# Kernel optimization log

Measured on AMD Instinct MI355X. Metric: run time of the kernel, lower is better.

The kernel has to match this reference:

```python
import jax, jax.numpy as jnp
import numpy as np

NUM_EXPERTS = 8
TOP_K = 2
HIDDEN = 1024
INTER = 3584
TOKENS = 16384


def setup_inputs() -> dict:
    key = jax.random.key(0)
    k0, k1, k2, k3, k4 = jax.random.split(key, 5)
    s = 0.02
    return {
        "hidden_states": jax.random.normal(k0, (TOKENS, HIDDEN), dtype=jnp.float32),
        "gate_w": jax.random.normal(k1, (NUM_EXPERTS, HIDDEN), dtype=jnp.float32) * s,
        "w1": jax.random.normal(k2, (NUM_EXPERTS, INTER, HIDDEN), dtype=jnp.float32) * s,
        "w3": jax.random.normal(k3, (NUM_EXPERTS, INTER, HIDDEN), dtype=jnp.float32) * s,
        "w2": jax.random.normal(k4, (NUM_EXPERTS, HIDDEN, INTER), dtype=jnp.float32) * s,
    }


def reference(hidden_states, gate_w, w1, w3, w2):
    # Router: logits -> softmax -> top-k -> renormalize (Mixtral gating)
    router_logits = jnp.einsum("th,eh->te", hidden_states, gate_w)  # [T, E]
    probs = jax.nn.softmax(router_logits, axis=-1)
    topk_w, topk_idx = jax.lax.top_k(probs, TOP_K)                  # [T, K]
    topk_w = topk_w / jnp.sum(topk_w, axis=-1, keepdims=True)
    # Dense combine weights: [T, E], zero for unselected experts
    combine = jnp.sum(
        jax.nn.one_hot(topk_idx, NUM_EXPERTS, dtype=hidden_states.dtype)
        * topk_w[..., None],
        axis=1,
    )
    out = jnp.zeros_like(hidden_states)
    for e in range(NUM_EXPERTS):  # small fixed expert loop
        h = jnp.einsum("th,ih->ti", hidden_states, w1[e])   # gate proj
        u = jnp.einsum("th,ih->ti", hidden_states, w3[e])   # up proj
        act = jax.nn.silu(h) * u                             # SwiGLU
        y = jnp.einsum("ti,hi->th", act, w2[e])              # down proj
        out = out + combine[:, e:e + 1] * y
    return out
```

## Files before the change

### kernel.cpp

```cpp
#include <hip/hip_runtime.h>
#include <hip/hip_bf16.h>

#define T_TOKENS 16384
#define HID 1024
#define NEXP 8
#define INTER 3584
#define PAIRS (2*T_TOKENS)
#define PAD_MAX (PAIRS + NEXP*256)

using f32x4    = __attribute__((ext_vector_type(4))) float;
using bfrag    = __attribute__((ext_vector_type(8))) short;
using float4_t = __attribute__((ext_vector_type(4))) float;
using ushort8_t = __attribute__((ext_vector_type(8))) unsigned short;

__device__ inline unsigned short f2bf(float f){
    unsigned u = __float_as_uint(f);
    u += 0x7FFFu + ((u >> 16) & 1u);
    return (unsigned short)(u >> 16);
}

__device__ inline void gload16(const unsigned short* g, unsigned short* l){
    __builtin_amdgcn_global_load_lds(
        (const __attribute__((address_space(1))) void*)g,
        (__attribute__((address_space(3))) void*)l, 16, 0, 0);
}

#define BAR_VM8() asm volatile("s_waitcnt vmcnt(8)\n\ts_barrier" ::: "memory")
#define BAR_VM4() asm volatile("s_waitcnt vmcnt(4)\n\ts_barrier" ::: "memory")
#define BAR_VM0() asm volatile("s_waitcnt vmcnt(0)\n\ts_barrier" ::: "memory")
#define BAR_PLAIN() asm volatile("s_barrier" ::: "memory")

__device__ inline int xcd_swz(int flat, int nwg){
    int q = nwg >> 3, r = nwg & 7;
    int xcd = flat & 7, idx = flat >> 3;
    return (xcd < r ? xcd*(q+1) : r*(q+1) + (xcd - r)*q) + idx;
}

__device__ inline void st_decode(int sw, int nM, int nP, int STM,
                                 int& mt, int& p){
    int stSize = STM * nP;
    int st = sw / stSize;
    int rem = sw - st * stSize;
    int base = st * STM;
    int stM = (base + STM <= nM) ? STM : (nM - base);
    p  = rem / stM;
    mt = base + (rem - p * stM);
}

__global__ __launch_bounds__(256) void conv3_kernel(
    const float* __restrict__ w1, const float* __restrict__ w3,
    const float* __restrict__ w2,
    unsigned short* __restrict__ w1b, unsigned short* __restrict__ w3b,
    unsigned short* __restrict__ w2b)
{
    const int n = NEXP * INTER * HID;
    const float* in = (blockIdx.y == 0) ? w1 : (blockIdx.y == 1) ? w3 : w2;
    unsigned short* out = (blockIdx.y == 0) ? w1b : (blockIdx.y == 1) ? w3b : w2b;
    int i0 = (blockIdx.x * 256 + threadIdx.x) * 8;
    int stride = gridDim.x * 256 * 8;
    for (int i = i0; i < n; i += stride){
        float4_t a = *reinterpret_cast<const float4_t*>(in + i);
        float4_t b = *reinterpret_cast<const float4_t*>(in + i + 4);
        ushort8_t o;
        o[0]=f2bf(a.x); o[1]=f2bf(a.y); o[2]=f2bf(a.z); o[3]=f2bf(a.w);
        o[4]=f2bf(b.x); o[5]=f2bf(b.y); o[6]=f2bf(b.z); o[7]=f2bf(b.w);
        *reinterpret_cast<ushort8_t*>(out + i) = o;
    }
}

__global__ __launch_bounds__(256) void router_kernel(
    const float* __restrict__ x, const float* __restrict__ gw,
    int* __restrict__ topk_idx, float* __restrict__ topk_w,
    unsigned short* __restrict__ xb)
{
    int wave = threadIdx.x >> 6;
    int lane = threadIdx.x & 63;
    int t = blockIdx.x * 4 + wave;

    float acc[NEXP];
#pragma unroll
    for (int e = 0; e < NEXP; ++e) acc[e] = 0.f;

    const float* xr = x + (size_t)t * HID;
    for (int hb = 0; hb < HID; hb += 64){
        float xv = xr[hb + lane];
#pragma unroll
        for (int e = 0; e < NEXP; ++e)
            acc[e] += xv * gw[e * HID + hb + lane];
    }

    unsigned short* xbr = xb + (size_t)t * HID;
#pragma unroll
    for (int r = 0; r < 2; ++r){
        int c = (lane + r*64) * 8;
        float4_t va = *reinterpret_cast<const float4_t*>(xr + c);
        float4_t vb = *reinterpret_cast<const float4_t*>(xr + c + 4);
        ushort8_t o;
        o[0]=f2bf(va.x); o[1]=f2bf(va.y); o[2]=f2bf(va.z); o[3]=f2bf(va.w);
        o[4]=f2bf(vb.x); o[5]=f2bf(vb.y); o[6]=f2bf(vb.z); o[7]=f2bf(vb.w);
        *reinterpret_cast<ushort8_t*>(xbr + c) = o;
    }

#pragma unroll
    for (int e = 0; e < NEXP; ++e){
#pragma unroll
        for (int s = 32; s > 0; s >>= 1)
            acc[e] += __shfl_xor(acc[e], s, 64);
    }
    if (lane == 0){
        int e0 = 0; float m0 = acc[0];
#pragma unroll
        for (int e = 1; e < NEXP; ++e) if (acc[e] > m0){ m0 = acc[e]; e0 = e; }
        int e1 = -1; float m1 = -1e30f;
#pragma unroll
        for (int e = 0; e < NEXP; ++e) if (e != e0 && acc[e] > m1){ m1 = acc[e]; e1 = e; }
        float p1 = __expf(m1 - m0);
        float inv = 1.f / (1.f + p1);
        topk_idx[2*t]   = e0;
        topk_idx[2*t+1] = e1;
        topk_w[2*t]   = inv;
        topk_w[2*t+1] = p1 * inv;
    }
}

__global__ __launch_bounds__(256) void hist_kernel(
    const int* __restrict__ topk_idx, int* __restrict__ counts)
{
    __shared__ int h[NEXP];
    if (threadIdx.x < NEXP) h[threadIdx.x] = 0;
    __syncthreads();
    int i0 = blockIdx.x * 256 + threadIdx.x;
    for (int i = i0; i < PAIRS; i += gridDim.x * 256)
        atomicAdd(&h[topk_idx[i]], 1);
    __syncthreads();
    if (threadIdx.x < NEXP) atomicAdd(&counts[threadIdx.x], h[threadIdx.x]);
}

__global__ void scan_kernel(const int* __restrict__ counts, int* __restrict__ offp)
{
    if (threadIdx.x == 0 && blockIdx.x == 0){
        int s = 0;
        for (int e = 0; e < NEXP; ++e){
            offp[e] = s;
            s += (counts[e] + 255) & ~255;
        }
        offp[NEXP] = s;
    }
}

__global__ __launch_bounds__(128) void padfill_kernel(
    const int* __restrict__ counts, const int* __restrict__ offp,
    int* __restrict__ pair_token, float* __restrict__ pair_w)
{
    int e = blockIdx.x;
    int base = offp[e];
    int aligned = offp[e+1] - base;
    for (int s = counts[e] + threadIdx.x; s < aligned; s += 128){
        pair_token[base + s] = (base + s) & (T_TOKENS - 1);
        pair_w[base + s] = 0.f;
    }
}

__global__ __launch_bounds__(256) void scatter_kernel(
    const int* __restrict__ topk_idx, const float* __restrict__ topk_w,
    const int* __restrict__ offp, int* __restrict__ cursors,
    int* __restrict__ pair_token, float* __restrict__ pair_w)
{
    __shared__ int hist[NEXP], base[NEXP], lcur[NEXP];
    int tid = threadIdx.x;
    if (tid < NEXP){ hist[tid] = 0; lcur[tid] = 0; }
    __syncthreads();

    int t = blockIdx.x * 256 + tid;
    int e0 = topk_idx[2*t], e1 = topk_idx[2*t + 1];
    atomicAdd(&hist[e0], 1);
    atomicAdd(&hist[e1], 1);
    __syncthreads();

    if (tid < NEXP) base[tid] = atomicAdd(&cursors[tid], hist[tid]);
    __syncthreads();

    int r0 = atomicAdd(&lcur[e0], 1);
    int r1 = atomicAdd(&lcur[e1], 1);
    int p0 = offp[e0] + base[e0] + r0;
    int p1 = offp[e1] + base[e1] + r1;
    pair_token[p0] = t;  pair_w[p0] = topk_w[2*t];
    pair_token[p1] = t;  pair_w[p1] = topk_w[2*t + 1];
}

__global__ __launch_bounds__(512) void gemm_act_kernel(
    const unsigned short* __restrict__ xb,
    const unsigned short* __restrict__ w1b,
    const unsigned short* __restrict__ w3b,
    const int* __restrict__ offp,
    const int* __restrict__ pair_token, const float* __restrict__ pair_w,
    unsigned short* __restrict__ act, int r0)
{
    int nP = gridDim.x, nM = gridDim.y;
    int sw = xcd_swz(blockIdx.y * nP + blockIdx.x, nP * nM);
    int mt, p;
    st_decode(sw, nM, nP, 4, mt, p);
    int by = mt, bx = p;

    int R = r0 + by * 256;
    if (R >= offp[NEXP]) return;
    int e = 0;
    while (offp[e+1] <= R) ++e;
    int icol0 = bx * 128;

    __shared__ alignas(16) unsigned short As0s[256*64], B1s0[128*64], B3s0[128*64];
    __shared__ alignas(16) unsigned short As1s[256*64], B1s1[128*64], B3s1[128*64];
    __shared__ int   toks[256];
    __shared__ float pws[256];

    int tid = threadIdx.x;
    if (tid < 256){
        toks[tid] = pair_token[R + tid];
        pws[tid]  = pair_w[R + tid];
    }
    __syncthreads();

    int w = tid >> 6, lane = tid & 63;
    int wm = w >> 2, wn = w & 3;
    int l15 = lane & 15;
    int sr = tid >> 3;
    int swzc8 = ((tid & 7) ^ (sr & 7)) * 8;

    const unsigned short* w1e = w1b + (size_t)e * INTER * HID;
    const unsigned short* w3e = w3b + (size_t)e * INTER * HID;

    size_t asrc[2][2];
#pragma unroll
    for (int h = 0; h < 2; ++h)
#pragma unroll
        for (int g = 0; g < 2; ++g)
            asrc[h][g] = (size_t)toks[h*128 + g*64 + sr] * HID + swzc8;
    size_t boff[2];
#pragma unroll
    for (int g = 0; g < 2; ++g)
        boff[g] = (size_t)(icol0 + g*64 + sr) * HID + swzc8;

    int ccol[2];
#pragma unroll
    for (int kk = 0; kk < 2; ++kk)
        ccol[kk] = (((kk*4 + (lane >> 4)) ^ (lane & 7)) * 8);

    f32x4 acc[8][4];
#pragma unroll
    for (int m = 0; m < 8; ++m)
#pragma unroll
        for (int n = 0; n < 4; ++n)
            acc[m][n] = (f32x4){0.f,0.f,0.f,0.f};

    bfrag asub[4][2];
    bfrag bsub[2][2];

    auto stA = [&](unsigned short* As, int h, int t){
        int kc = t * 64;
        gload16(xb + asrc[h][0] + kc, As + h*8192 + tid*8);
        gload16(xb + asrc[h][1] + kc, As + h*8192 + 4096 + tid*8);
    };
    auto stBh = [&](unsigned short* B1s, int t){
        int kc = t * 64;
        gload16(w1e + boff[0] + kc, B1s + tid*8);
        gload16(w1e + boff[1] + kc, B1s + 4096 + tid*8);
    };
    auto stBu = [&](unsigned short* B3s, int t){
        int kc = t * 64;
        gload16(w3e + boff[0] + kc, B3s + tid*8);
        gload16(w3e + boff[1] + kc, B3s + 4096 + tid*8);
    };

    auto dsA = [&](const unsigned short* As, int Mh){
#pragma unroll
        for (int mfl = 0; mfl < 4; ++mfl)
#pragma unroll
            for (int kk = 0; kk < 2; ++kk)
                asub[mfl][kk] = *reinterpret_cast<const bfrag*>(
                    &As[(Mh*128 + wm*64 + mfl*16 + l15)*64 + ccol[kk]]);
    };
    auto dsB = [&](const unsigned short* Bs){
#pragma unroll
        for (int nf = 0; nf < 2; ++nf)
#pragma unroll
            for (int kk = 0; kk < 2; ++kk)
                bsub[nf][kk] = *reinterpret_cast<const bfrag*>(
                    &Bs[(wn*32 + nf*16 + l15)*64 + ccol[kk]]);
    };
    auto mma = [&](int Mh, int S){
        __builtin_amdgcn_s_setprio(1);
#pragma unroll
        for (int kk = 0; kk < 2; ++kk)
#pragma unroll
            for (int nf = 0; nf < 2; ++nf)
#pragma unroll
                for (int mfl = 0; mfl < 4; ++mfl)
                    acc[Mh*4+mfl][S*2+nf] = __builtin_amdgcn_mfma_f32_16x16x32_bf16(
                        asub[mfl][kk], bsub[nf][kk], acc[Mh*4+mfl][S*2+nf], 0, 0, 0);
        __builtin_amdgcn_s_setprio(0);
    };

    const int NT = HID / 64;

    stBh(B1s0, 0);
    stA(As0s, 1, 0);
    stA(As0s, 0, 0);
    stBu(B3s0, 0);
    stBh(B1s1, 1);
    stA(As1s, 1, 1);
    BAR_VM4();

#pragma unroll 1
    for (int i = 0; i < NT/2 - 1; ++i){
        int t1 = 2*i + 1, t2 = 2*i + 2, t3 = 2*i + 3;
        dsA(As0s, 0); dsB(B1s0);
        stA(As1s, 0, t1);
        BAR_PLAIN(); mma(0, 0); BAR_PLAIN();
        dsA(As0s, 1);
        stBu(B3s1, t1);
        BAR_PLAIN(); mma(1, 0); BAR_PLAIN();
        dsB(B3s0);
        stBh(B1s0, t2);
        BAR_PLAIN(); mma(1, 1); BAR_PLAIN();
        dsA(As0s, 0);
        stA(As0s, 1, t2);
        BAR_VM4(); mma(0, 1); BAR_PLAIN();
        dsA(As1s, 0); dsB(B1s1);
        stA(As0s, 0, t2);
        BAR_PLAIN(); mma(0, 0); BAR_PLAIN();
        dsA(As1s, 1);
        stBu(B3s0, t2);
        BAR_PLAIN(); mma(1, 0); BAR_PLAIN();
        dsB(B3s1);
        stBh(B1s1, t3);
        BAR_PLAIN(); mma(1, 1); BAR_PLAIN();
        dsA(As1s, 0);
        stA(As1s, 1, t3);
        BAR_VM4(); mma(0, 1); BAR_PLAIN();
    }

    dsA(As0s, 0); dsB(B1s0);
    stA(As1s, 0, NT-1);
    BAR_PLAIN(); mma(0, 0); BAR_PLAIN();
    dsA(As0s, 1);
    stBu(B3s1, NT-1);
    BAR_PLAIN(); mma(1, 0); BAR_PLAIN();
    dsB(B3s0);
    BAR_PLAIN(); mma(1, 1); BAR_PLAIN();
    dsA(As0s, 0);
    BAR_VM0(); mma(0, 1); BAR_PLAIN();
    dsA(As1s, 0); dsB(B1s1);
    BAR_PLAIN(); mma(0, 0); BAR_PLAIN();
    dsA(As1s, 1);
    BAR_PLAIN(); mma(1, 0); BAR_PLAIN();
    dsB(B3s1);
    BAR_PLAIN(); mma(1, 1); BAR_PLAIN();
    dsA(As1s, 0);
    BAR_PLAIN(); mma(0, 1); BAR_PLAIN();

    size_t arow0 = (size_t)(by * 256) * INTER;
#pragma unroll
    for (int m = 0; m < 8; ++m){
#pragma unroll
        for (int nf = 0; nf < 2; ++nf){
#pragma unroll
            for (int j = 0; j < 4; ++j){
                int rl = (m >> 2)*128 + wm*64 + (m & 3)*16 + (lane >> 4)*4 + j;
                float h = acc[m][nf][j];
                float u = acc[m][2 + nf][j];
                float v = pws[rl] * h * u / (1.f + __expf(-h));
                int ic = icol0 + wn*32 + nf*16 + l15;
                act[arow0 + (size_t)rl * INTER + ic] = f2bf(v);
            }
        }
    }
}

__global__ __launch_bounds__(256) void gemm2_kernel(
    const unsigned short* __restrict__ act,
    const unsigned short* __restrict__ w2b,
    const int* __restrict__ offp,
    const int* __restrict__ pair_token,
    float* __restrict__ out, int r0)
{
    int nP = gridDim.x, nM = gridDim.y;
    int sw = xcd_swz(blockIdx.y * nP + blockIdx.x, nP * nM);
    int mt, p;
    st_decode(sw, nM, nP, 4, mt, p);
    int by = mt, bx = p;

    int R = r0 + by * 128;
    if (R >= offp[NEXP]) return;
    int e = 0;
    while (offp[e+1] <= R) ++e;
    int h0 = bx * 128;

    __shared__ alignas(16) unsigned short As0[128*64], As1[128*64];
    __shared__ alignas(16) unsigned short Bs0[128*64], Bs1[128*64];
    __shared__ int toks[128];

    int tid = threadIdx.x;
    if (tid < 128) toks[tid] = pair_token[R + tid];
    __syncthreads();

    int w = tid >> 6, lane = tid & 63;
    int wm = w >> 1, wn = w & 1;
    int lr = lane >> 3;
    int l15 = lane & 15;
    int swz8 = ((lane & 7) ^ lr) * 8;

    const unsigned short* w2e = w2b + (size_t)e * HID * INTER;
    size_t arow0 = (size_t)(by * 128) * INTER;

    size_t asrc[4], bsrc[4];
#pragma unroll
    for (int i = 0; i < 4; ++i){
        asrc[i] = arow0 + (size_t)(w*32 + i*8 + lr) * INTER + swz8;
        bsrc[i] = (size_t)(h0 + w*32 + i*8 + lr) * INTER + swz8;
    }

    int ccol[2];
#pragma unroll
    for (int kk = 0; kk < 2; ++kk)
        ccol[kk] = (((kk*4 + (lane >> 4)) ^ (lane & 7)) * 8);

    f32x4 acc[4][4];
#pragma unroll
    for (int m = 0; m < 4; ++m)
#pragma unroll
        for (int n = 0; n < 4; ++n)
            acc[m][n] = (f32x4){0.f,0.f,0.f,0.f};

    auto stageT = [&](unsigned short* As, unsigned short* Bs, int t){
        int kc = t * 64;
#pragma unroll
        for (int i = 0; i < 4; ++i) gload16(act + asrc[i] + kc, As + (w*32 + i*8)*64);
#pragma unroll
        for (int i = 0; i < 4; ++i) gload16(w2e + bsrc[i] + kc, Bs + (w*32 + i*8)*64);
    };

    auto computeT = [&](const unsigned short* As, const unsigned short* Bs){
        __builtin_amdgcn_s_setprio(1);
#pragma unroll
        for (int kk = 0; kk < 2; ++kk){
            int cc = ccol[kk];
            bfrag a[4];
#pragma unroll
            for (int m = 0; m < 4; ++m)
                a[m] = *reinterpret_cast<const bfrag*>(&As[(wm*64 + m*16 + l15)*64 + cc]);
#pragma unroll
            for (int n = 0; n < 4; ++n){
                bfrag b = *reinterpret_cast<const bfrag*>(&Bs[(wn*64 + n*16 + l15)*64 + cc]);
#pragma unroll
                for (int m = 0; m < 4; ++m)
                    acc[m][n] = __builtin_amdgcn_mfma_f32_16x16x32_bf16(a[m], b, acc[m][n], 0, 0, 0);
            }
        }
        __builtin_amdgcn_s_setprio(0);
    };

    const int NT = INTER / 64;
    stageT(As0, Bs0, 0);
    stageT(As1, Bs1, 1);
#pragma unroll 1
    for (int t = 0; t < NT - 2; t += 2){
        BAR_VM8();
        computeT(As0, Bs0);
        BAR_PLAIN();
        stageT(As0, Bs0, t + 2);
        BAR_VM8();
        computeT(As1, Bs1);
        BAR_PLAIN();
        stageT(As1, Bs1, t + 3);
    }
    BAR_VM8();
    computeT(As0, Bs0);
    BAR_VM0();
    computeT(As1, Bs1);

#pragma unroll
    for (int m = 0; m < 4; ++m){
#pragma unroll
        for (int n = 0; n < 4; ++n){
#pragma unroll
            for (int j = 0; j < 4; ++j){
                int rl = wm*64 + m*16 + (lane >> 4)*4 + j;
                int hc = h0 + wn*64 + n*16 + l15;
                atomicAdd(&out[(size_t)toks[rl] * HID + hc], acc[m][n][j]);
            }
        }
    }
}

extern "C" void kernel_launch(void* const* d_in, const int* in_sizes, int n_in,
                              void* d_out, int out_size, void* d_ws, size_t ws_size,
                              hipStream_t stream)
{
    const float* x  = (const float*)d_in[0];
    const float* gw = (const float*)d_in[1];
    const float* w1 = (const float*)d_in[2];
    const float* w3 = (const float*)d_in[3];
    const float* w2 = (const float*)d_in[4];
    float* out = (float*)d_out;

    char* ws = (char*)d_ws;
    size_t off = 0;
    auto bump = [&](size_t bytes) -> void* {
        void* p = ws + off;
        off = (off + bytes + 255) & ~(size_t)255;
        return p;
    };
    int*   counts     = (int*)bump(32);
    int*   cursors    = (int*)bump(32);
    int*   offp       = (int*)bump(64);
    int*   topk_idx   = (int*)bump((size_t)PAIRS * 4);
    float* topk_w     = (float*)bump((size_t)PAIRS * 4);
    int*   pair_token = (int*)bump((size_t)PAD_MAX * 4);
    float* pair_w     = (float*)bump((size_t)PAD_MAX * 4);
    unsigned short* xb  = (unsigned short*)bump((size_t)T_TOKENS * HID * 2);
    unsigned short* w1b = (unsigned short*)bump((size_t)NEXP * INTER * HID * 2);
    unsigned short* w3b = (unsigned short*)bump((size_t)NEXP * INTER * HID * 2);
    unsigned short* w2b = (unsigned short*)bump((size_t)NEXP * HID * INTER * 2);
    unsigned short* act = (unsigned short*)(ws + off);

    size_t rem = (ws_size > off) ? (ws_size - off) : 0;
    int RC = (int)(rem / ((size_t)INTER * 2));
    RC &= ~255;
    if (RC > PAD_MAX) RC = PAD_MAX;
    if (RC < 256) RC = 256;
    int nchunks = (PAD_MAX + RC - 1) / RC;

    hipMemsetAsync(d_out, 0, (size_t)T_TOKENS * HID * 4, stream);
    hipMemsetAsync(ws, 0, 1024, stream);

    conv3_kernel<<<dim3(768, 3), 256, 0, stream>>>(w1, w3, w2, w1b, w3b, w2b);

    router_kernel<<<T_TOKENS/4, 256, 0, stream>>>(x, gw, topk_idx, topk_w, xb);
    hist_kernel<<<64, 256, 0, stream>>>(topk_idx, counts);
    scan_kernel<<<1, 64, 0, stream>>>(counts, offp);
    padfill_kernel<<<NEXP, 128, 0, stream>>>(counts, offp, pair_token, pair_w);
    scatter_kernel<<<T_TOKENS/256, 256, 0, stream>>>(topk_idx, topk_w, offp, cursors,
                                                     pair_token, pair_w);

    for (int c = 0; c < nchunks; ++c){
        int r0 = c * RC;
        gemm_act_kernel<<<dim3(INTER/128, RC/256), 512, 0, stream>>>(
            xb, w1b, w3b, offp, pair_token, pair_w, act, r0);
        gemm2_kernel<<<dim3(HID/128, RC/128), 256, 0, stream>>>(
            act, w2b, offp, pair_token, out, r0);
    }
}
```

Before: 1.089 ms.

## Triple-buffer both MoE GEMMs and retile gemm2 to 256-row 512-thread blocks

The gate/up GEMM now uses 256x64 output tiles, with the h and u accumulators kept separate. Its K-loop runs a three-stage LDS ring with a uniform per-tile schedule instead of the hand-interleaved double-buffer sequence. The down-projection GEMM moves from 128x128 tiles with 256 threads to 256x128 tiles with 512 threads and the same three-stage ring, which halves the number of row blocks reloading W2. Deeper prefetch is meant to hide global-load latency better, at the cost of more LDS per block (lower occupancy) and, for the first GEMM, twice as many column blocks re-reading the gathered activations.

```diff
diff --git a/kernel.cpp b/kernel.cpp
--- a/kernel.cpp
+++ b/kernel.cpp
@@ -25,8 +25,7 @@
         (__attribute__((address_space(3))) void*)l, 16, 0, 0);
 }
 
-#define BAR_VM8() asm volatile("s_waitcnt vmcnt(8)\n\ts_barrier" ::: "memory")
-#define BAR_VM4() asm volatile("s_waitcnt vmcnt(4)\n\ts_barrier" ::: "memory")
+#define BAR_VM6() asm volatile("s_waitcnt vmcnt(6)\n\ts_barrier" ::: "memory")
 #define BAR_VM0() asm volatile("s_waitcnt vmcnt(0)\n\ts_barrier" ::: "memory")
 #define BAR_PLAIN() asm volatile("s_barrier" ::: "memory")
 
@@ -206,10 +205,11 @@
     if (R >= offp[NEXP]) return;
     int e = 0;
     while (offp[e+1] <= R) ++e;
-    int icol0 = bx * 128;
-
-    __shared__ alignas(16) unsigned short As0s[256*64], B1s0[128*64], B3s0[128*64];
-    __shared__ alignas(16) unsigned short As1s[256*64], B1s1[128*64], B3s1[128*64];
+    int icol0 = bx * 64;
+
+    __shared__ alignas(16) unsigned short A0[256*64], A1[256*64], A2[256*64];
+    __shared__ alignas(16) unsigned short B10[64*64], B11[64*64], B12[64*64];
+    __shared__ alignas(16) unsigned short B30[64*64], B31[64*64], B32[64*64];
     __shared__ int   toks[256];
     __shared__ float pws[256];
 
@@ -235,148 +235,105 @@
 #pragma unroll
         for (int g = 0; g < 2; ++g)
             asrc[h][g] = (size_t)toks[h*128 + g*64 + sr] * HID + swzc8;
-    size_t boff[2];
-#pragma unroll
-    for (int g = 0; g < 2; ++g)
-        boff[g] = (size_t)(icol0 + g*64 + sr) * HID + swzc8;
+    size_t bsrc = (size_t)(icol0 + sr) * HID + swzc8;
 
     int ccol[2];
 #pragma unroll
     for (int kk = 0; kk < 2; ++kk)
         ccol[kk] = (((kk*4 + (lane >> 4)) ^ (lane & 7)) * 8);
 
-    f32x4 acc[8][4];
-#pragma unroll
-    for (int m = 0; m < 8; ++m)
-#pragma unroll
-        for (int n = 0; n < 4; ++n)
-            acc[m][n] = (f32x4){0.f,0.f,0.f,0.f};
+    f32x4 acc_h[8], acc_u[8];
+#pragma unroll
+    for (int m = 0; m < 8; ++m){
+        acc_h[m] = (f32x4){0.f,0.f,0.f,0.f};
+        acc_u[m] = (f32x4){0.f,0.f,0.f,0.f};
+    }
 
     bfrag asub[4][2];
-    bfrag bsub[2][2];
-
-    auto stA = [&](unsigned short* As, int h, int t){
-        int kc = t * 64;
-        gload16(xb + asrc[h][0] + kc, As + h*8192 + tid*8);
-        gload16(xb + asrc[h][1] + kc, As + h*8192 + 4096 + tid*8);
-    };
-    auto stBh = [&](unsigned short* B1s, int t){
-        int kc = t * 64;
-        gload16(w1e + boff[0] + kc, B1s + tid*8);
-        gload16(w1e + boff[1] + kc, B1s + 4096 + tid*8);
-    };
-    auto stBu = [&](unsigned short* B3s, int t){
-        int kc = t * 64;
-        gload16(w3e + boff[0] + kc, B3s + tid*8);
-        gload16(w3e + boff[1] + kc, B3s + 4096 + tid*8);
-    };
-
-    auto dsA = [&](const unsigned short* As, int Mh){
-#pragma unroll
-        for (int mfl = 0; mfl < 4; ++mfl)
+    bfrag bh[2], bu[2];
+
+    auto stA = [&](unsigned short* A, int h, int t){
+        int k0 = t * 64;
+        gload16(xb + asrc[h][0] + k0, A + h*8192 + tid*8);
+        gload16(xb + asrc[h][1] + k0, A + h*8192 + 4096 + tid*8);
+    };
+    auto stB = [&](unsigned short* B1, unsigned short* B3, int t){
+        int k0 = t * 64;
+        gload16(w1e + bsrc + k0, B1 + tid*8);
+        gload16(w3e + bsrc + k0, B3 + tid*8);
+    };
+
+    auto dsA = [&](const unsigned short* A, int q){
+#pragma unroll
+        for (int i = 0; i < 4; ++i)
 #pragma unroll
             for (int kk = 0; kk < 2; ++kk)
-                asub[mfl][kk] = *reinterpret_cast<const bfrag*>(
-                    &As[(Mh*128 + wm*64 + mfl*16 + l15)*64 + ccol[kk]]);
-    };
-    auto dsB = [&](const unsigned short* Bs){
-#pragma unroll
-        for (int nf = 0; nf < 2; ++nf)
-#pragma unroll
-            for (int kk = 0; kk < 2; ++kk)
-                bsub[nf][kk] = *reinterpret_cast<const bfrag*>(
-                    &Bs[(wn*32 + nf*16 + l15)*64 + ccol[kk]]);
-    };
-    auto mma = [&](int Mh, int S){
+                asub[i][kk] = *reinterpret_cast<const bfrag*>(
+                    &A[(wm*128 + q*64 + i*16 + l15)*64 + ccol[kk]]);
+    };
+    auto dsB = [&](const unsigned short* B1, const unsigned short* B3){
+#pragma unroll
+        for (int kk = 0; kk < 2; ++kk){
+            bh[kk] = *reinterpret_cast<const bfrag*>(&B1[(wn*16 + l15)*64 + ccol[kk]]);
+            bu[kk] = *reinterpret_cast<const bfrag*>(&B3[(wn*16 + l15)*64 + ccol[kk]]);
+        }
+    };
+    auto mma = [&](int q){
         __builtin_amdgcn_s_setprio(1);
 #pragma unroll
         for (int kk = 0; kk < 2; ++kk)
 #pragma unroll
-            for (int nf = 0; nf < 2; ++nf)
-#pragma unroll
-                for (int mfl = 0; mfl < 4; ++mfl)
-                    acc[Mh*4+mfl][S*2+nf] = __builtin_amdgcn_mfma_f32_16x16x32_bf16(
-                        asub[mfl][kk], bsub[nf][kk], acc[Mh*4+mfl][S*2+nf], 0, 0, 0);
+            for (int i = 0; i < 4; ++i){
+                acc_h[q*4+i] = __builtin_amdgcn_mfma_f32_16x16x32_bf16(asub[i][kk], bh[kk], acc_h[q*4+i], 0, 0, 0);
+                acc_u[q*4+i] = __builtin_amdgcn_mfma_f32_16x16x32_bf16(asub[i][kk], bu[kk], acc_u[q*4+i], 0, 0, 0);
+            }
         __builtin_amdgcn_s_setprio(0);
     };
 
-    const int NT = HID / 64;
-
-    stBh(B1s0, 0);
-    stA(As0s, 1, 0);
-    stA(As0s, 0, 0);
-    stBu(B3s0, 0);
-    stBh(B1s1, 1);
-    stA(As1s, 1, 1);
-    BAR_VM4();
+    auto TILE = [&](const unsigned short* Xa, const unsigned short* Xb1, const unsigned short* Xb3,
+                    unsigned short* Ya, unsigned short* Yb1, unsigned short* Yb3,
+                    int tn, int mode){
+        dsA(Xa, 0); dsB(Xb1, Xb3);
+        if (mode == 0){ stA(Ya, 0, tn); stA(Ya, 1, tn); }
+        BAR_PLAIN(); mma(0); BAR_PLAIN();
+        dsA(Xa, 1);
+        if (mode == 0) stB(Yb1, Yb3, tn);
+        if (mode == 0) BAR_VM6();
+        else if (mode == 1) BAR_VM0();
+        else BAR_PLAIN();
+        mma(1); BAR_PLAIN();
+    };
+
+    stA(A0, 0, 0); stA(A0, 1, 0); stB(B10, B30, 0);
+    stA(A1, 0, 1); stA(A1, 1, 1); stB(B11, B31, 1);
+    BAR_VM6();
 
 #pragma unroll 1
-    for (int i = 0; i < NT/2 - 1; ++i){
-        int t1 = 2*i + 1, t2 = 2*i + 2, t3 = 2*i + 3;
-        dsA(As0s, 0); dsB(B1s0);
-        stA(As1s, 0, t1);
-        BAR_PLAIN(); mma(0, 0); BAR_PLAIN();
-        dsA(As0s, 1);
-        stBu(B3s1, t1);
-        BAR_PLAIN(); mma(1, 0); BAR_PLAIN();
-        dsB(B3s0);
-        stBh(B1s0, t2);
-        BAR_PLAIN(); mma(1, 1); BAR_PLAIN();
-        dsA(As0s, 0);
-        stA(As0s, 1, t2);
-        BAR_VM4(); mma(0, 1); BAR_PLAIN();
-        dsA(As1s, 0); dsB(B1s1);
-        stA(As0s, 0, t2);
-        BAR_PLAIN(); mma(0, 0); BAR_PLAIN();
-        dsA(As1s, 1);
-        stBu(B3s0, t2);
-        BAR_PLAIN(); mma(1, 0); BAR_PLAIN();
-        dsB(B3s1);
-        stBh(B1s1, t3);
-        BAR_PLAIN(); mma(1, 1); BAR_PLAIN();
-        dsA(As1s, 0);
-        stA(As1s, 1, t3);
-        BAR_VM4(); mma(0, 1); BAR_PLAIN();
-    }
-
-    dsA(As0s, 0); dsB(B1s0);
-    stA(As1s, 0, NT-1);
-    BAR_PLAIN(); mma(0, 0); BAR_PLAIN();
-    dsA(As0s, 1);
-    stBu(B3s1, NT-1);
-    BAR_PLAIN(); mma(1, 0); BAR_PLAIN();
-    dsB(B3s0);
-    BAR_PLAIN(); mma(1, 1); BAR_PLAIN();
-    dsA(As0s, 0);
-    BAR_VM0(); mma(0, 1); BAR_PLAIN();
-    dsA(As1s, 0); dsB(B1s1);
-    BAR_PLAIN(); mma(0, 0); BAR_PLAIN();
-    dsA(As1s, 1);
-    BAR_PLAIN(); mma(1, 0); BAR_PLAIN();
-    dsB(B3s1);
-    BAR_PLAIN(); mma(1, 1); BAR_PLAIN();
-    dsA(As1s, 0);
-    BAR_PLAIN(); mma(0, 1); BAR_PLAIN();
+    for (int g = 0; g < 4; ++g){
+        TILE(A0, B10, B30, A2, B12, B32, 3*g + 2, 0);
+        TILE(A1, B11, B31, A0, B10, B30, 3*g + 3, 0);
+        TILE(A2, B12, B32, A1, B11, B31, 3*g + 4, 0);
+    }
+    TILE(A0, B10, B30, A2, B12, B32, 14, 0);
+    TILE(A1, B11, B31, A0, B10, B30, 15, 0);
+    TILE(A2, B12, B32, A0, B10, B30, 0, 1);
+    TILE(A0, B10, B30, A0, B10, B30, 0, 2);
 
     size_t arow0 = (size_t)(by * 256) * INTER;
 #pragma unroll
     for (int m = 0; m < 8; ++m){
 #pragma unroll
-        for (int nf = 0; nf < 2; ++nf){
-#pragma unroll
-            for (int j = 0; j < 4; ++j){
-                int rl = (m >> 2)*128 + wm*64 + (m & 3)*16 + (lane >> 4)*4 + j;
-                float h = acc[m][nf][j];
-                float u = acc[m][2 + nf][j];
-                float v = pws[rl] * h * u / (1.f + __expf(-h));
-                int ic = icol0 + wn*32 + nf*16 + l15;
-                act[arow0 + (size_t)rl * INTER + ic] = f2bf(v);
-            }
+        for (int j = 0; j < 4; ++j){
+            int rl = wm*128 + m*16 + (lane >> 4)*4 + j;
+            float h = acc_h[m][j];
+            float u = acc_u[m][j];
+            float v = pws[rl] * h * u / (1.f + __expf(-h));
+            act[arow0 + (size_t)rl * INTER + icol0 + wn*16 + l15] = f2bf(v);
         }
     }
 }
 
-__global__ __launch_bounds__(256) void gemm2_kernel(
+__global__ __launch_bounds__(512) void gemm2_kernel(
     const unsigned short* __restrict__ act,
     const unsigned short* __restrict__ w2b,
     const int* __restrict__ offp,
@@ -386,107 +343,133 @@
     int nP = gridDim.x, nM = gridDim.y;
     int sw = xcd_swz(blockIdx.y * nP + blockIdx.x, nP * nM);
     int mt, p;
-    st_decode(sw, nM, nP, 4, mt, p);
+    st_decode(sw, nM, nP, 2, mt, p);
     int by = mt, bx = p;
 
-    int R = r0 + by * 128;
+    int R = r0 + by * 256;
     if (R >= offp[NEXP]) return;
     int e = 0;
     while (offp[e+1] <= R) ++e;
     int h0 = bx * 128;
 
-    __shared__ alignas(16) unsigned short As0[128*64], As1[128*64];
-    __shared__ alignas(16) unsigned short Bs0[128*64], Bs1[128*64];
-    __shared__ int toks[128];
+    __shared__ alignas(16) unsigned short A0[256*64], A1[256*64], A2[256*64];
+    __shared__ alignas(16) unsigned short B0[128*64], B1[128*64], B2[128*64];
+    __shared__ int toks[256];
 
     int tid = threadIdx.x;
-    if (tid < 128) toks[tid] = pair_token[R + tid];
+    if (tid < 256) toks[tid] = pair_token[R + tid];
     __syncthreads();
 
     int w = tid >> 6, lane = tid & 63;
-    int wm = w >> 1, wn = w & 1;
-    int lr = lane >> 3;
+    int wm = w >> 2, wn = w & 3;
     int l15 = lane & 15;
-    int swz8 = ((lane & 7) ^ lr) * 8;
+    int sr = tid >> 3;
+    int swzc8 = ((tid & 7) ^ (sr & 7)) * 8;
 
     const unsigned short* w2e = w2b + (size_t)e * HID * INTER;
-    size_t arow0 = (size_t)(by * 128) * INTER;
-
-    size_t asrc[4], bsrc[4];
-#pragma unroll
-    for (int i = 0; i < 4; ++i){
-        asrc[i] = arow0 + (size_t)(w*32 + i*8 + lr) * INTER + swz8;
-        bsrc[i] = (size_t)(h0 + w*32 + i*8 + lr) * INTER + swz8;
-    }
+    size_t arow0 = (size_t)(by * 256) * INTER;
+
+    size_t asrc[2][2];
+#pragma unroll
+    for (int h = 0; h < 2; ++h)
+#pragma unroll
+        for (int g = 0; g < 2; ++g)
+            asrc[h][g] = arow0 + (size_t)(h*128 + g*64 + sr) * INTER + swzc8;
+    size_t bsrc[2];
+#pragma unroll
+    for (int g = 0; g < 2; ++g)
+        bsrc[g] = (size_t)(h0 + g*64 + sr) * INTER + swzc8;
 
     int ccol[2];
 #pragma unroll
     for (int kk = 0; kk < 2; ++kk)
         ccol[kk] = (((kk*4 + (lane >> 4)) ^ (lane & 7)) * 8);
 
-    f32x4 acc[4][4];
-#pragma unroll
-    for (int m = 0; m < 4; ++m)
-#pragma unroll
-        for (int n = 0; n < 4; ++n)
+    f32x4 acc[8][2];
+#pragma unroll
+    for (int m = 0; m < 8; ++m)
+#pragma unroll
+        for (int n = 0; n < 2; ++n)
             acc[m][n] = (f32x4){0.f,0.f,0.f,0.f};
 
-    auto stageT = [&](unsigned short* As, unsigned short* Bs, int t){
+    bfrag asub[4][2];
+    bfrag bsub[2][2];
+
+    auto stA = [&](unsigned short* A, int h, int t){
         int kc = t * 64;
-#pragma unroll
-        for (int i = 0; i < 4; ++i) gload16(act + asrc[i] + kc, As + (w*32 + i*8)*64);
-#pragma unroll
-        for (int i = 0; i < 4; ++i) gload16(w2e + bsrc[i] + kc, Bs + (w*32 + i*8)*64);
-    };
-
-    auto computeT = [&](const unsigned short* As, const unsigned short* Bs){
+        gload16(act + asrc[h][0] + kc, A + h*8192 + tid*8);
+        gload16(act + asrc[h][1] + kc, A + h*8192 + 4096 + tid*8);
+    };
+    auto stB = [&](unsigned short* B, int t){
+        int kc = t * 64;
+        gload16(w2e + bsrc[0] + kc, B + tid*8);
+        gload16(w2e + bsrc[1] + kc, B + 4096 + tid*8);
+    };
+
+    auto dsA = [&](const unsigned short* A, int q){
+#pragma unroll
+        for (int i = 0; i < 4; ++i)
+#pragma unroll
+            for (int kk = 0; kk < 2; ++kk)
+                asub[i][kk] = *reinterpret_cast<const bfrag*>(
+                    &A[(wm*128 + q*64 + i*16 + l15)*64 + ccol[kk]]);
+    };
+    auto dsB = [&](const unsigned short* B){
+#pragma unroll
+        for (int nf = 0; nf < 2; ++nf)
+#pragma unroll
+            for (int kk = 0; kk < 2; ++kk)
+                bsub[nf][kk] = *reinterpret_cast<const bfrag*>(
+                    &B[(wn*32 + nf*16 + l15)*64 + ccol[kk]]);
+    };
+    auto mma = [&](int q){
         __builtin_amdgcn_s_setprio(1);
 #pragma unroll
-        for (int kk = 0; kk < 2; ++kk){
-            int cc = ccol[kk];
-            bfrag a[4];
-#pragma unroll
-            for (int m = 0; m < 4; ++m)
-                a[m] = *reinterpret_cast<const bfrag*>(&As[(wm*64 + m*16 + l15)*64 + cc]);
-#pragma unroll
-            for (int n = 0; n < 4; ++n){
-                bfrag b = *reinterpret_cast<const bfrag*>(&Bs[(wn*64 + n*16 + l15)*64 + cc]);
-#pragma unroll
-                for (int m = 0; m < 4; ++m)
-                    acc[m][n] = __builtin_amdgcn_mfma_f32_16x16x32_bf16(a[m], b, acc[m][n], 0, 0, 0);
-            }
-        }
+        for (int kk = 0; kk < 2; ++kk)
+#pragma unroll
+            for (int nf = 0; nf < 2; ++nf)
+#pragma unroll
+                for (int i = 0; i < 4; ++i)
+                    acc[q*4+i][nf] = __builtin_amdgcn_mfma_f32_16x16x32_bf16(
+                        asub[i][kk], bsub[nf][kk], acc[q*4+i][nf], 0, 0, 0);
         __builtin_amdgcn_s_setprio(0);
     };
 
-    const int NT = INTER / 64;
-    stageT(As0, Bs0, 0);
-    stageT(As1, Bs1, 1);
+    auto TILE = [&](const unsigned short* Xa, const unsigned short* Xb,
+                    unsigned short* Ya, unsigned short* Yb, int tn, int mode){
+        dsA(Xa, 0); dsB(Xb);
+        if (mode == 0){ stA(Ya, 0, tn); stA(Ya, 1, tn); }
+        BAR_PLAIN(); mma(0); BAR_PLAIN();
+        dsA(Xa, 1);
+        if (mode == 0) stB(Yb, tn);
+        if (mode == 0) BAR_VM6();
+        else if (mode == 1) BAR_VM0();
+        else BAR_PLAIN();
+        mma(1); BAR_PLAIN();
+    };
+
+    stA(A0, 0, 0); stA(A0, 1, 0); stB(B0, 0);
+    stA(A1, 0, 1); stA(A1, 1, 1); stB(B1, 1);
+    BAR_VM6();
+
 #pragma unroll 1
-    for (int t = 0; t < NT - 2; t += 2){
-        BAR_VM8();
-        computeT(As0, Bs0);
-        BAR_PLAIN();
-        stageT(As0, Bs0, t + 2);
-        BAR_VM8();
-        computeT(As1, Bs1);
-        BAR_PLAIN();
-        stageT(As1, Bs1, t + 3);
-    }
-    BAR_VM8();
-    computeT(As0, Bs0);
-    BAR_VM0();
-    computeT(As1, Bs1);
-
-#pragma unroll
-    for (int m = 0; m < 4; ++m){
-#pragma unroll
-        for (int n = 0; n < 4; ++n){
+    for (int g = 0; g < 18; ++g){
+        TILE(A0, B0, A2, B2, 3*g + 2, 0);
+        TILE(A1, B1, A0, B0, 3*g + 3, 0);
+        TILE(A2, B2, A1, B1, 3*g + 4, 0);
+    }
+    TILE(A0, B0, A0, B0, 0, 1);
+    TILE(A1, B1, A0, B0, 0, 2);
+
+#pragma unroll
+    for (int m = 0; m < 8; ++m){
+#pragma unroll
+        for (int nf = 0; nf < 2; ++nf){
 #pragma unroll
             for (int j = 0; j < 4; ++j){
-                int rl = wm*64 + m*16 + (lane >> 4)*4 + j;
-                int hc = h0 + wn*64 + n*16 + l15;
-                atomicAdd(&out[(size_t)toks[rl] * HID + hc], acc[m][n][j]);
+                int rl = wm*128 + m*16 + (lane >> 4)*4 + j;
+                int hc = h0 + wn*32 + nf*16 + l15;
+                atomicAdd(&out[(size_t)toks[rl] * HID + hc], acc[m][nf][j]);
             }
         }
     }
@@ -544,9 +527,9 @@
 
     for (int c = 0; c < nchunks; ++c){
         int r0 = c * RC;
-        gemm_act_kernel<<<dim3(INTER/128, RC/256), 512, 0, stream>>>(
+        gemm_act_kernel<<<dim3(INTER/64, RC/256), 512, 0, stream>>>(
             xb, w1b, w3b, offp, pair_token, pair_w, act, r0);
-        gemm2_kernel<<<dim3(HID/128, RC/128), 256, 0, stream>>>(
+        gemm2_kernel<<<dim3(HID/128, RC/256), 512, 0, stream>>>(
             act, w2b, offp, pair_token, out, r0);
     }
 }
```

Measured after the change: 1.242 ms. +14.0%, slower.

## Restructure gate/up GEMM pipeline into whole-tile double-buffered stages

Applied to the files above, without the earlier changes.

Replaces the fine-grained interleaved staging in the gate/up GEMM kernel with a simpler scheme: each K-tile's A, W1 and W3 slices go into one of two full buffers. The next-but-one tile is issued after three of the four MFMA phases, and a vmcnt(8) barrier waits only for the following tile. Warp rows now map to contiguous 128-row blocks, and B fragments for gate and up are held separately. This cuts repeated A-fragment LDS reloads per tile and simplifies barrier placement. The cost is a larger burst of global loads at a single point and a different overlap pattern, which could expose more memory latency.

```diff
diff --git a/kernel.cpp b/kernel.cpp
--- a/kernel.cpp
+++ b/kernel.cpp
@@ -26,7 +26,6 @@
 }
 
 #define BAR_VM8() asm volatile("s_waitcnt vmcnt(8)\n\ts_barrier" ::: "memory")
-#define BAR_VM4() asm volatile("s_waitcnt vmcnt(4)\n\ts_barrier" ::: "memory")
 #define BAR_VM0() asm volatile("s_waitcnt vmcnt(0)\n\ts_barrier" ::: "memory")
 #define BAR_PLAIN() asm volatile("s_barrier" ::: "memory")
 
@@ -208,8 +207,9 @@
     while (offp[e+1] <= R) ++e;
     int icol0 = bx * 128;
 
-    __shared__ alignas(16) unsigned short As0s[256*64], B1s0[128*64], B3s0[128*64];
-    __shared__ alignas(16) unsigned short As1s[256*64], B1s1[128*64], B3s1[128*64];
+    __shared__ alignas(16) unsigned short A0[256*64], A1[256*64];
+    __shared__ alignas(16) unsigned short B10[128*64], B11[128*64];
+    __shared__ alignas(16) unsigned short B30[128*64], B31[128*64];
     __shared__ int   toks[256];
     __shared__ float pws[256];
 
@@ -229,16 +229,14 @@
     const unsigned short* w1e = w1b + (size_t)e * INTER * HID;
     const unsigned short* w3e = w3b + (size_t)e * INTER * HID;
 
-    size_t asrc[2][2];
-#pragma unroll
-    for (int h = 0; h < 2; ++h)
-#pragma unroll
-        for (int g = 0; g < 2; ++g)
-            asrc[h][g] = (size_t)toks[h*128 + g*64 + sr] * HID + swzc8;
-    size_t boff[2];
+    size_t asrc[4];
+#pragma unroll
+    for (int g = 0; g < 4; ++g)
+        asrc[g] = (size_t)toks[g*64 + sr] * HID + swzc8;
+    size_t bsrc[2];
 #pragma unroll
     for (int g = 0; g < 2; ++g)
-        boff[g] = (size_t)(icol0 + g*64 + sr) * HID + swzc8;
+        bsrc[g] = (size_t)(icol0 + g*64 + sr) * HID + swzc8;
 
     int ccol[2];
 #pragma unroll
@@ -252,111 +250,96 @@
         for (int n = 0; n < 4; ++n)
             acc[m][n] = (f32x4){0.f,0.f,0.f,0.f};
 
-    bfrag asub[4][2];
-    bfrag bsub[2][2];
-
-    auto stA = [&](unsigned short* As, int h, int t){
-        int kc = t * 64;
-        gload16(xb + asrc[h][0] + kc, As + h*8192 + tid*8);
-        gload16(xb + asrc[h][1] + kc, As + h*8192 + 4096 + tid*8);
-    };
-    auto stBh = [&](unsigned short* B1s, int t){
-        int kc = t * 64;
-        gload16(w1e + boff[0] + kc, B1s + tid*8);
-        gload16(w1e + boff[1] + kc, B1s + 4096 + tid*8);
-    };
-    auto stBu = [&](unsigned short* B3s, int t){
-        int kc = t * 64;
-        gload16(w3e + boff[0] + kc, B3s + tid*8);
-        gload16(w3e + boff[1] + kc, B3s + 4096 + tid*8);
-    };
-
-    auto dsA = [&](const unsigned short* As, int Mh){
-#pragma unroll
-        for (int mfl = 0; mfl < 4; ++mfl)
+    bfrag a[4][2];
+    bfrag bh[2][2], bu[2][2];
+
+    auto stageAll = [&](unsigned short* A, unsigned short* B1, unsigned short* B3, int t){
+        int k0 = t * 64;
+        gload16(xb  + asrc[0] + k0, A + tid*8);
+        gload16(xb  + asrc[1] + k0, A + 4096 + tid*8);
+        gload16(xb  + asrc[2] + k0, A + 8192 + tid*8);
+        gload16(xb  + asrc[3] + k0, A + 12288 + tid*8);
+        gload16(w1e + bsrc[0] + k0, B1 + tid*8);
+        gload16(w1e + bsrc[1] + k0, B1 + 4096 + tid*8);
+        gload16(w3e + bsrc[0] + k0, B3 + tid*8);
+        gload16(w3e + bsrc[1] + k0, B3 + 4096 + tid*8);
+    };
+
+    auto dsA = [&](const unsigned short* A, int q){
+#pragma unroll
+        for (int i = 0; i < 4; ++i)
 #pragma unroll
             for (int kk = 0; kk < 2; ++kk)
-                asub[mfl][kk] = *reinterpret_cast<const bfrag*>(
-                    &As[(Mh*128 + wm*64 + mfl*16 + l15)*64 + ccol[kk]]);
-    };
-    auto dsB = [&](const unsigned short* Bs){
+                a[i][kk] = *reinterpret_cast<const bfrag*>(
+                    &A[(wm*128 + q*64 + i*16 + l15)*64 + ccol[kk]]);
+    };
+    auto dsBh = [&](const unsigned short* B1){
 #pragma unroll
         for (int nf = 0; nf < 2; ++nf)
 #pragma unroll
             for (int kk = 0; kk < 2; ++kk)
-                bsub[nf][kk] = *reinterpret_cast<const bfrag*>(
-                    &Bs[(wn*32 + nf*16 + l15)*64 + ccol[kk]]);
-    };
-    auto mma = [&](int Mh, int S){
+                bh[nf][kk] = *reinterpret_cast<const bfrag*>(
+                    &B1[(wn*32 + nf*16 + l15)*64 + ccol[kk]]);
+    };
+    auto dsBu = [&](const unsigned short* B3){
+#pragma unroll
+        for (int nf = 0; nf < 2; ++nf)
+#pragma unroll
+            for (int kk = 0; kk < 2; ++kk)
+                bu[nf][kk] = *reinterpret_cast<const bfrag*>(
+                    &B3[(wn*32 + nf*16 + l15)*64 + ccol[kk]]);
+    };
+    auto mma = [&](int q, int s){
         __builtin_amdgcn_s_setprio(1);
-#pragma unroll
-        for (int kk = 0; kk < 2; ++kk)
-#pragma unroll
-            for (int nf = 0; nf < 2; ++nf)
-#pragma unroll
-                for (int mfl = 0; mfl < 4; ++mfl)
-                    acc[Mh*4+mfl][S*2+nf] = __builtin_amdgcn_mfma_f32_16x16x32_bf16(
-                        asub[mfl][kk], bsub[nf][kk], acc[Mh*4+mfl][S*2+nf], 0, 0, 0);
+        if (s == 0){
+#pragma unroll
+            for (int kk = 0; kk < 2; ++kk)
+#pragma unroll
+                for (int nf = 0; nf < 2; ++nf)
+#pragma unroll
+                    for (int i = 0; i < 4; ++i)
+                        acc[q*4+i][nf] = __builtin_amdgcn_mfma_f32_16x16x32_bf16(
+                            a[i][kk], bh[nf][kk], acc[q*4+i][nf], 0, 0, 0);
+        } else {
+#pragma unroll
+            for (int kk = 0; kk < 2; ++kk)
+#pragma unroll
+                for (int nf = 0; nf < 2; ++nf)
+#pragma unroll
+                    for (int i = 0; i < 4; ++i)
+                        acc[q*4+i][2+nf] = __builtin_amdgcn_mfma_f32_16x16x32_bf16(
+                            a[i][kk], bu[nf][kk], acc[q*4+i][2+nf], 0, 0, 0);
+        }
         __builtin_amdgcn_s_setprio(0);
     };
 
+    auto TILE = [&](const unsigned short* A, const unsigned short* B1, const unsigned short* B3,
+                    unsigned short* Aw, unsigned short* B1w, unsigned short* B3w,
+                    int tn, int mode){
+        dsA(A, 0); dsBh(B1);
+        BAR_PLAIN(); mma(0, 0); BAR_PLAIN();
+        dsBu(B3);
+        BAR_PLAIN(); mma(0, 1); BAR_PLAIN();
+        dsA(A, 1);
+        BAR_PLAIN(); mma(1, 1); BAR_PLAIN();
+        if (mode == 0){ stageAll(Aw, B1w, B3w, tn); BAR_VM8(); }
+        else if (mode == 1){ BAR_VM0(); }
+        else { BAR_PLAIN(); }
+        mma(1, 0);
+    };
+
     const int NT = HID / 64;
-
-    stBh(B1s0, 0);
-    stA(As0s, 1, 0);
-    stA(As0s, 0, 0);
-    stBu(B3s0, 0);
-    stBh(B1s1, 1);
-    stA(As1s, 1, 1);
-    BAR_VM4();
+    stageAll(A0, B10, B30, 0);
+    stageAll(A1, B11, B31, 1);
+    BAR_VM8();
 
 #pragma unroll 1
-    for (int i = 0; i < NT/2 - 1; ++i){
-        int t1 = 2*i + 1, t2 = 2*i + 2, t3 = 2*i + 3;
-        dsA(As0s, 0); dsB(B1s0);
-        stA(As1s, 0, t1);
-        BAR_PLAIN(); mma(0, 0); BAR_PLAIN();
-        dsA(As0s, 1);
-        stBu(B3s1, t1);
-        BAR_PLAIN(); mma(1, 0); BAR_PLAIN();
-        dsB(B3s0);
-        stBh(B1s0, t2);
-        BAR_PLAIN(); mma(1, 1); BAR_PLAIN();
-        dsA(As0s, 0);
-        stA(As0s, 1, t2);
-        BAR_VM4(); mma(0, 1); BAR_PLAIN();
-        dsA(As1s, 0); dsB(B1s1);
-        stA(As0s, 0, t2);
-        BAR_PLAIN(); mma(0, 0); BAR_PLAIN();
-        dsA(As1s, 1);
-        stBu(B3s0, t2);
-        BAR_PLAIN(); mma(1, 0); BAR_PLAIN();
-        dsB(B3s1);
-        stBh(B1s1, t3);
-        BAR_PLAIN(); mma(1, 1); BAR_PLAIN();
-        dsA(As1s, 0);
-        stA(As1s, 1, t3);
-        BAR_VM4(); mma(0, 1); BAR_PLAIN();
-    }
-
-    dsA(As0s, 0); dsB(B1s0);
-    stA(As1s, 0, NT-1);
-    BAR_PLAIN(); mma(0, 0); BAR_PLAIN();
-    dsA(As0s, 1);
-    stBu(B3s1, NT-1);
-    BAR_PLAIN(); mma(1, 0); BAR_PLAIN();
-    dsB(B3s0);
-    BAR_PLAIN(); mma(1, 1); BAR_PLAIN();
-    dsA(As0s, 0);
-    BAR_VM0(); mma(0, 1); BAR_PLAIN();
-    dsA(As1s, 0); dsB(B1s1);
-    BAR_PLAIN(); mma(0, 0); BAR_PLAIN();
-    dsA(As1s, 1);
-    BAR_PLAIN(); mma(1, 0); BAR_PLAIN();
-    dsB(B3s1);
-    BAR_PLAIN(); mma(1, 1); BAR_PLAIN();
-    dsA(As1s, 0);
-    BAR_PLAIN(); mma(0, 1); BAR_PLAIN();
+    for (int t = 0; t < NT - 2; t += 2){
+        TILE(A0, B10, B30, A0, B10, B30, t + 2, 0);
+        TILE(A1, B11, B31, A1, B11, B31, t + 3, 0);
+    }
+    TILE(A0, B10, B30, A0, B10, B30, 0, 1);
+    TILE(A1, B11, B31, A1, B11, B31, 0, 2);
 
     size_t arow0 = (size_t)(by * 256) * INTER;
 #pragma unroll
@@ -365,7 +348,7 @@
         for (int nf = 0; nf < 2; ++nf){
 #pragma unroll
             for (int j = 0; j < 4; ++j){
-                int rl = (m >> 2)*128 + wm*64 + (m & 3)*16 + (lane >> 4)*4 + j;
+                int rl = wm*128 + m*16 + (lane >> 4)*4 + j;
                 float h = acc[m][nf][j];
                 float u = acc[m][2 + nf][j];
                 float v = pws[rl] * h * u / (1.f + __expf(-h));
```

Result: faster. 1.044 ms (-4.2%).
